# Performance work log

Measured on AMD Instinct MI355X. Metric: run time of the kernel, lower is better.

## Reference

```python
import jax, jax.numpy as jnp
import numpy as np

B, S, I, H, O, E, K = 2, 2048, 4096, 1376, 4096, 8, 2
BALANCE_W = 0.01  # balance_loss_weight in llama-moe


def setup_inputs() -> dict:
    key = jax.random.key(0)
    ks = jax.random.split(key, 6)
    sc = lambda k, shape, fan: jax.random.normal(k, shape, jnp.float32) * (fan ** -0.5)
    return {
        "x": jax.random.normal(ks[0], (B, S, I), jnp.float32),
        "gate_w": sc(ks[1], (E, I), I),          # linear gate network, no bias
        "w_gate": sc(ks[2], (E, H, I), I),       # GLU gate proj per expert
        "b_gate": jnp.zeros((E, H), jnp.float32),
        "w_up": sc(ks[3], (E, H, I), I),         # GLU up proj per expert
        "b_up": jnp.zeros((E, H), jnp.float32),
        "w_down": sc(ks[4], (E, O, H), H),       # down proj per expert
        "b_down": jnp.zeros((E, O), jnp.float32),
    }


def _cv_squared(v, eps=1e-10):
    # torch: x.var() / (x.mean()**2 + eps), unbiased variance
    mean = jnp.mean(v)
    var = jnp.sum((v - mean) ** 2) / (v.shape[0] - 1)
    return var / (mean ** 2 + eps)


def reference(x, gate_w, w_gate, b_gate, w_up, b_up, w_down, b_down):
    bsz, seq, _ = x.shape
    xt = x.reshape(-1, I)                         # [T, I] tokens
    T = xt.shape[0]

    # ---- TopKBalancedNoisyGate (no-noise branch) ----
    logits = xt @ gate_w.T                        # [T, E]
    top_logits, top_idx = jax.lax.top_k(logits, K)
    top_scores = jax.nn.softmax(top_logits, axis=-1)   # softmax over top-k logits
    # dense routing matrix: zeros.scatter(1, top_idx, top_scores)
    dense = jnp.zeros((T, E), xt.dtype).at[jnp.arange(T)[:, None], top_idx].set(top_scores)
    importance = dense.sum(axis=0)                # [E]
    load = (dense > 0).astype(jnp.float32).sum(axis=0)  # [E]
    gate_loss = BALANCE_W * (_cv_squared(importance) + _cv_squared(load))

    # ---- UniversalCalculator over LinearGLUExperts ----
    # Dense-dispatch formulation: compute every expert on every token, weight by
    # the (mostly-zero) routing matrix -> identical math to gather/grouped-GEMM/scatter.
    g = jnp.einsum('ti,ehi->teh', xt, w_gate) + b_gate        # [T, E, H]
    u = jnp.einsum('ti,ehi->teh', xt, w_up) + b_up            # [T, E, H]
    inter = jax.nn.silu(g) * u                                # GLU
    # score * (W_down h + b_down) == W_down (score*h) + score*b_down
    y = jnp.einsum('teh,eoh->to', inter * dense[:, :, None], w_down) + dense @ b_down
    return y.reshape(bsz, seq, O), gate_loss
```

## Files before the change

kernel.cpp:

```cpp
#include <hip/hip_runtime.h>
#include <hip/hip_bf16.h>
#include <stdint.h>

#define TN 4096
#define DI 4096
#define DH 1376
#define DHP 1408
#define DO 4096
#define NE 8
#define NPAIR 8192

typedef unsigned short u16;
typedef __bf16 bf16x8 __attribute__((ext_vector_type(8)));
typedef float f32x4 __attribute__((ext_vector_type(4)));
typedef uint32_t u32x4 __attribute__((ext_vector_type(4)));

__device__ __forceinline__ uint32_t pack2bf(float a, float b) {
    union { float f; uint32_t u; } ua, ub;
    ua.f = a; ub.f = b;
    uint32_t lo = (ua.u + 0x7fffu + ((ua.u >> 16) & 1u)) >> 16;
    uint32_t hi = (ub.u + 0x7fffu + ((ub.u >> 16) & 1u)) >> 16;
    return lo | (hi << 16);
}
__device__ __forceinline__ u16 f2bf(float a) {
    union { float f; uint32_t u; } ua; ua.f = a;
    return (u16)((ua.u + 0x7fffu + ((ua.u >> 16) & 1u)) >> 16);
}
__device__ __forceinline__ void gload16(const void* g, void* l) {
    __builtin_amdgcn_global_load_lds(
        (const __attribute__((address_space(1))) void*)g,
        (__attribute__((address_space(3))) void*)l, 16, 0, 0);
}
#define MEMFENCE() asm volatile("" ::: "memory")

__global__ __launch_bounds__(256) void k_cvt(const float* __restrict__ src,
                                             u16* __restrict__ dst, int n8)
{
    int i = blockIdx.x * 256 + threadIdx.x;
    if (i >= n8) return;
    const float4* s = (const float4*)(src + (size_t)i * 8);
    float4 a = s[0], b = s[1];
    u32x4 q = {pack2bf(a.x, a.y), pack2bf(a.z, a.w), pack2bf(b.x, b.y), pack2bf(b.z, b.w)};
    *(u32x4*)(dst + (size_t)i * 8) = q;
}

__global__ __launch_bounds__(256) void k_cvt_wd(const float* __restrict__ src,
                                                u16* __restrict__ dst)
{
    int i = blockIdx.x * 256 + threadIdx.x;
    int row = i / 176, c8 = (i % 176) * 8;
    u32x4 q = {0u, 0u, 0u, 0u};
    if (c8 < DH) {
        const float4* s = (const float4*)(src + (size_t)row * DH + c8);
        float4 a = s[0], b = s[1];
        q = (u32x4){pack2bf(a.x, a.y), pack2bf(a.z, a.w), pack2bf(b.x, b.y), pack2bf(b.z, b.w)};
    }
    *(u32x4*)(dst + (size_t)row * DHP + c8) = q;
}

__global__ __launch_bounds__(256) void k_gate(
    const float* __restrict__ x, const float* __restrict__ gw,
    u16* __restrict__ x16, int* __restrict__ tke, float* __restrict__ tks,
    int* __restrict__ cnt, float* __restrict__ imp)
{
    int t = blockIdx.x, tid = threadIdx.x;
    const float* xr = x + (size_t)t * DI;
    double acc[NE];
#pragma unroll
    for (int e = 0; e < NE; ++e) acc[e] = 0.0;
#pragma unroll
    for (int j = 0; j < 4; ++j) {
        int i4 = (j * 256 + tid) * 4;
        float4 xv = *(const float4*)(xr + i4);
        uint2 p; p.x = pack2bf(xv.x, xv.y); p.y = pack2bf(xv.z, xv.w);
        *(uint2*)(x16 + (size_t)t * DI + i4) = p;
#pragma unroll
        for (int e = 0; e < NE; ++e) {
            float4 wv = *(const float4*)(gw + (size_t)e * DI + i4);
            acc[e] = fma((double)xv.x, (double)wv.x, acc[e]);
            acc[e] = fma((double)xv.y, (double)wv.y, acc[e]);
            acc[e] = fma((double)xv.z, (double)wv.z, acc[e]);
            acc[e] = fma((double)xv.w, (double)wv.w, acc[e]);
        }
    }
#pragma unroll
    for (int o = 32; o > 0; o >>= 1)
#pragma unroll
        for (int e = 0; e < NE; ++e) acc[e] += __shfl_down(acc[e], o, 64);
    __shared__ double lred[4][NE];
    if ((tid & 63) == 0)
#pragma unroll
        for (int e = 0; e < NE; ++e) lred[tid >> 6][e] = acc[e];
    __syncthreads();
    if (tid == 0) {
        double lg[NE];
#pragma unroll
        for (int e = 0; e < NE; ++e) lg[e] = lred[0][e] + lred[1][e] + lred[2][e] + lred[3][e];
        int e1 = 0;
        for (int e = 1; e < NE; ++e) if (lg[e] > lg[e1]) e1 = e;
        int e2 = -1;
        for (int e = 0; e < NE; ++e) { if (e == e1) continue; if (e2 < 0 || lg[e] > lg[e2]) e2 = e; }
        float d = (float)(lg[e2] - lg[e1]);
        float ed = expf(d);
        float s1 = 1.0f / (1.0f + ed);
        float s2 = ed / (1.0f + ed);
        tke[2 * t] = e1; tke[2 * t + 1] = e2;
        tks[2 * t] = s1; tks[2 * t + 1] = s2;
        atomicAdd(&cnt[e1], 1); atomicAdd(&cnt[e2], 1);
        unsafeAtomicAdd(&imp[e1], s1); unsafeAtomicAdd(&imp[e2], s2);
    }
}

__global__ void k_finalize(const int* __restrict__ cnt, const float* __restrict__ imp,
                           int* __restrict__ off, float* __restrict__ loss_out)
{
    if (threadIdx.x == 0 && blockIdx.x == 0) {
        int o = 0;
        for (int e = 0; e < NE; ++e) { off[e] = o; o += cnt[e]; }
        float m1 = 0.f, m2 = 0.f;
        for (int e = 0; e < NE; ++e) { m1 += imp[e]; m2 += (float)cnt[e]; }
        m1 *= 0.125f; m2 *= 0.125f;
        float v1 = 0.f, v2 = 0.f;
        for (int e = 0; e < NE; ++e) {
            float d1 = imp[e] - m1, d2 = (float)cnt[e] - m2;
            v1 += d1 * d1; v2 += d2 * d2;
        }
        v1 /= 7.0f; v2 /= 7.0f;
        float cv1 = v1 / (m1 * m1 + 1e-10f);
        float cv2 = v2 / (m2 * m2 + 1e-10f);
        *loss_out = 0.01f * (cv1 + cv2);
    }
}

__global__ __launch_bounds__(256) void k_scatter(
    const int* __restrict__ tke, const float* __restrict__ tks,
    const int* __restrict__ off, int* __restrict__ fill,
    int* __restrict__ tok, float* __restrict__ sc)
{
    int t = blockIdx.x * 256 + threadIdx.x;
    if (t >= TN) return;
#pragma unroll
    for (int k = 0; k < 2; ++k) {
        int e = tke[2 * t + k];
        int pos = off[e] + atomicAdd(&fill[e], 1);
        tok[pos] = t; sc[pos] = tks[2 * t + k];
    }
}

__global__ __launch_bounds__(256) void k_yinit(
    const int* __restrict__ tke, const float* __restrict__ tks,
    const float* __restrict__ bd, float* __restrict__ y)
{
    int t = blockIdx.x, tid = threadIdx.x;
    int e1 = tke[2 * t], e2 = tke[2 * t + 1];
    float s1 = tks[2 * t], s2 = tks[2 * t + 1];
    const float4* b1 = (const float4*)(bd + (size_t)e1 * DO);
    const float4* b2 = (const float4*)(bd + (size_t)e2 * DO);
    float4* yr = (float4*)(y + (size_t)t * DO);
#pragma unroll
    for (int j = 0; j < 4; ++j) {
        int i = j * 256 + tid;
        float4 a = b1[i], b = b2[i], r;
        r.x = s1 * a.x + s2 * b.x; r.y = s1 * a.y + s2 * b.y;
        r.z = s1 * a.z + s2 * b.z; r.w = s1 * a.w + s2 * b.w;
        yr[i] = r;
    }
}


__global__ __launch_bounds__(256, 2) void k_stage1g(
    const u16* __restrict__ x16,
    const u16* __restrict__ wg16, const u16* __restrict__ wu16,
    const float* __restrict__ bg, const float* __restrict__ bu,
    const int* __restrict__ cnt, const int* __restrict__ off,
    const int* __restrict__ tok, const float* __restrict__ sc,
    u16* __restrict__ inter)
{
    int e = blockIdx.x & 7;
    int ce = cnt[e];
    int rows0 = (blockIdx.x >> 3) * 128;
    if (rows0 >= ce) return;
    int oe = off[e];
    int h0 = blockIdx.y * 128;
    int tid = threadIdx.x;

    __shared__ u16 As0[128 * 32]; __shared__ u16 As1[128 * 32]; __shared__ u16 As2[128 * 32];
    __shared__ u16 Gs0[128 * 32]; __shared__ u16 Gs1[128 * 32]; __shared__ u16 Gs2[128 * 32];
    __shared__ u16 Us0[128 * 32]; __shared__ u16 Us1[128 * 32]; __shared__ u16 Us2[128 * 32];

    int swz = ((tid & 3) ^ ((tid >> 3) & 3)) * 8;
    const u16* ab0; const u16* ab1; const u16* gb0; const u16* gb1;
    const u16* ub0; const u16* ub1;
    {
        int rl0 = tid >> 2, rl1 = 64 + (tid >> 2);
        int rg0 = oe + min(rows0 + rl0, ce - 1);
        int rg1 = oe + min(rows0 + rl1, ce - 1);
        ab0 = x16 + (size_t)tok[rg0] * DI + swz;
        ab1 = x16 + (size_t)tok[rg1] * DI + swz;
        int hr0 = min(h0 + rl0, DH - 1), hr1 = min(h0 + rl1, DH - 1);
        gb0 = wg16 + ((size_t)e * DH + hr0) * DI + swz;
        gb1 = wg16 + ((size_t)e * DH + hr1) * DI + swz;
        ub0 = wu16 + ((size_t)e * DH + hr0) * DI + swz;
        ub1 = wu16 + ((size_t)e * DH + hr1) * DI + swz;
    }

    int wid = tid >> 6, lane = tid & 63;
    int ldsw = wid * 512;
    int wm = wid >> 1, wn = wid & 1;
    int rA = wm * 64 + (lane & 15);
    int rB = wn * 64 + (lane & 15);
    int colb = (((lane >> 4) ^ ((lane >> 1) & 3)) & 3) * 8;

    f32x4 accg[4][4], accu[4][4];
    f32x4 vz = {0.f, 0.f, 0.f, 0.f};
#pragma unroll
    for (int m = 0; m < 4; ++m)
#pragma unroll
        for (int n = 0; n < 4; ++n) { accg[m][n] = vz; accu[m][n] = vz; }

#define S1_STAGE(A_, G_, U_, K0)                                   \
    do {                                                           \
        gload16(ab0 + (K0), &A_[ldsw]);                            \
        gload16(ab1 + (K0), &A_[2048 + ldsw]);                     \
        gload16(gb0 + (K0), &G_[ldsw]);                            \
        gload16(gb1 + (K0), &G_[2048 + ldsw]);                     \
        gload16(ub0 + (K0), &U_[ldsw]);                            \
        gload16(ub1 + (K0), &U_[2048 + ldsw]);                     \
    } while (0)

#define S1_COMPUTE(A_, G_, U_)                                     \
    do {                                                           \
        bf16x8 a[4], g[4], u[4];                                   \
        _Pragma("unroll")                                          \
        for (int m = 0; m < 4; ++m)                                \
            a[m] = *(const bf16x8*)&A_[(rA + m * 16) * 32 + colb]; \
        _Pragma("unroll")                                          \
        for (int n = 0; n < 4; ++n) {                              \
            g[n] = *(const bf16x8*)&G_[(rB + n * 16) * 32 + colb]; \
            u[n] = *(const bf16x8*)&U_[(rB + n * 16) * 32 + colb]; \
        }                                                          \
        __builtin_amdgcn_s_setprio(1);                             \
        _Pragma("unroll")                                          \
        for (int m = 0; m < 4; ++m)                                \
            _Pragma("unroll")                                      \
            for (int n = 0; n < 4; ++n) {                          \
                accg[m][n] = __builtin_amdgcn_mfma_f32_16x16x32_bf16(a[m], g[n], accg[m][n], 0, 0, 0); \
                accu[m][n] = __builtin_amdgcn_mfma_f32_16x16x32_bf16(a[m], u[n], accu[m][n], 0, 0, 0); \
            }                                                      \
        __builtin_amdgcn_s_setprio(0);                             \
    } while (0)

#define S1_PHASE(A_, G_, U_, KN)                                   \
    do {                                                           \
        asm volatile("s_waitcnt vmcnt(12)" ::: "memory");          \
        __builtin_amdgcn_s_barrier();                              \
        MEMFENCE();                                                \
        S1_COMPUTE(A_, G_, U_);                                    \
        __builtin_amdgcn_s_barrier();                              \
        MEMFENCE();                                                \
        S1_STAGE(A_, G_, U_, KN);                                  \
    } while (0)

    const int NT = DI / 32;
    const int KL = (NT - 1) * 32;
    S1_STAGE(As0, Gs0, Us0, 0);
    S1_STAGE(As1, Gs1, Us1, 32);
    S1_STAGE(As2, Gs2, Us2, 64);

    for (int kt = 0; kt + 4 < NT; kt += 3) {
        S1_PHASE(As0, Gs0, Us0, min((kt + 3) * 32, KL));
        S1_PHASE(As1, Gs1, Us1, min((kt + 4) * 32, KL));
        S1_PHASE(As2, Gs2, Us2, min((kt + 5) * 32, KL));
    }
    asm volatile("s_waitcnt vmcnt(12)" ::: "memory");
    __builtin_amdgcn_s_barrier();
    MEMFENCE();
    S1_COMPUTE(As0, Gs0, Us0);
    asm volatile("s_waitcnt vmcnt(6)" ::: "memory");
    __builtin_amdgcn_s_barrier();
    MEMFENCE();
    S1_COMPUTE(As1, Gs1, Us1);
    asm volatile("s_waitcnt vmcnt(0)" ::: "memory");
#undef S1_STAGE
#undef S1_COMPUTE
#undef S1_PHASE

    int rmax = ce - rows0;
    float bgv[4], buv[4];
    int hc[4]; bool hok[4];
#pragma unroll
    for (int n = 0; n < 4; ++n) {
        hc[n] = h0 + wn * 64 + n * 16 + (lane & 15);
        hok[n] = hc[n] < DH;
        bgv[n] = hok[n] ? bg[e * DH + hc[n]] : 0.f;
        buv[n] = hok[n] ? bu[e * DH + hc[n]] : 0.f;
    }
#pragma unroll
    for (int m = 0; m < 4; ++m) {
#pragma unroll
        for (int r = 0; r < 4; ++r) {
            int rl = wm * 64 + m * 16 + (lane >> 4) * 4 + r;
            if (rl < rmax) {
                int rg = oe + rows0 + rl;
                float s = sc[rg];
                size_t rowb = (size_t)rg * DHP;
#pragma unroll
                for (int n = 0; n < 4; ++n) {
                    float v = 0.f;
                    if (hok[n]) {
                        float gv = accg[m][n][r] + bgv[n];
                        float uv = accu[m][n][r] + buv[n];
                        float sig = 1.0f / (1.0f + __expf(-gv));
                        v = s * gv * sig * uv;
                    }
                    inter[rowb + hc[n]] = f2bf(v);
                }
            }
        }
    }
}

__global__ __launch_bounds__(256, 2) void k_stage2g(
    const u16* __restrict__ inter, const u16* __restrict__ wd16,
    const int* __restrict__ cnt, const int* __restrict__ off,
    const int* __restrict__ tok, float* __restrict__ y)
{
    int e = blockIdx.x & 7;
    int ce = cnt[e];
    int rows0 = (blockIdx.x >> 3) * 128;
    if (rows0 >= ce) return;
    int oe = off[e];
    int o0 = blockIdx.y * 128;
    int tid = threadIdx.x;

    __shared__ u16 As0[128 * 32]; __shared__ u16 As1[128 * 32]; __shared__ u16 As2[128 * 32];
    __shared__ u16 Bs0[128 * 32]; __shared__ u16 Bs1[128 * 32]; __shared__ u16 Bs2[128 * 32];

    int swz = ((tid & 3) ^ ((tid >> 3) & 3)) * 8;
    const u16* ab0; const u16* ab1; const u16* bb0; const u16* bb1;
    {
        int rl0 = tid >> 2, rl1 = 64 + (tid >> 2);
        int ar0 = min(oe + rows0 + rl0, NPAIR - 1);
        int ar1 = min(oe + rows0 + rl1, NPAIR - 1);
        ab0 = inter + (size_t)ar0 * DHP + swz;
        ab1 = inter + (size_t)ar1 * DHP + swz;
        bb0 = wd16 + ((size_t)e * DO + (o0 + rl0)) * DHP + swz;
        bb1 = wd16 + ((size_t)e * DO + (o0 + rl1)) * DHP + swz;
    }

    int wid = tid >> 6, lane = tid & 63;
    int ldsw = wid * 512;
    int wm = wid >> 1, wn = wid & 1;
    int rA = wm * 64 + (lane & 15);
    int rB = wn * 64 + (lane & 15);
    int colb = (((lane >> 4) ^ ((lane >> 1) & 3)) & 3) * 8;

    f32x4 acc[4][4];
    f32x4 vz = {0.f, 0.f, 0.f, 0.f};
#pragma unroll
    for (int m = 0; m < 4; ++m)
#pragma unroll
        for (int n = 0; n < 4; ++n) acc[m][n] = vz;

#define S2_STAGE(A_, B_, K0)                                       \
    do {                                                           \
        gload16(ab0 + (K0), &A_[ldsw]);                            \
        gload16(ab1 + (K0), &A_[2048 + ldsw]);                     \
        gload16(bb0 + (K0), &B_[ldsw]);                            \
        gload16(bb1 + (K0), &B_[2048 + ldsw]);                     \
    } while (0)

#define S2_COMPUTE(A_, B_)                                         \
    do {                                                           \
        bf16x8 a[4], b[4];                                         \
        _Pragma("unroll")                                          \
        for (int m = 0; m < 4; ++m)                                \
            a[m] = *(const bf16x8*)&A_[(rA + m * 16) * 32 + colb]; \
        _Pragma("unroll")                                          \
        for (int n = 0; n < 4; ++n)                                \
            b[n] = *(const bf16x8*)&B_[(rB + n * 16) * 32 + colb]; \
        __builtin_amdgcn_s_setprio(1);                             \
        _Pragma("unroll")                                          \
        for (int m = 0; m < 4; ++m)                                \
            _Pragma("unroll")                                      \
            for (int n = 0; n < 4; ++n)                            \
                acc[m][n] = __builtin_amdgcn_mfma_f32_16x16x32_bf16(a[m], b[n], acc[m][n], 0, 0, 0); \
        __builtin_amdgcn_s_setprio(0);                             \
    } while (0)

#define S2_PHASE(A_, B_, KN)                                       \
    do {                                                           \
        asm volatile("s_waitcnt vmcnt(8)" ::: "memory");           \
        __builtin_amdgcn_s_barrier();                              \
        MEMFENCE();                                                \
        S2_COMPUTE(A_, B_);                                        \
        __builtin_amdgcn_s_barrier();                              \
        MEMFENCE();                                                \
        S2_STAGE(A_, B_, KN);                                      \
    } while (0)

    const int NT = DHP / 32;
    const int KL = (NT - 1) * 32;
    S2_STAGE(As0, Bs0, 0);
    S2_STAGE(As1, Bs1, 32);
    S2_STAGE(As2, Bs2, 64);

    for (int kt = 0; kt + 4 < NT; kt += 3) {
        S2_PHASE(As0, Bs0, min((kt + 3) * 32, KL));
        S2_PHASE(As1, Bs1, min((kt + 4) * 32, KL));
        S2_PHASE(As2, Bs2, min((kt + 5) * 32, KL));
    }
    asm volatile("s_waitcnt vmcnt(8)" ::: "memory");
    __builtin_amdgcn_s_barrier();
    MEMFENCE();
    S2_COMPUTE(As0, Bs0);
    asm volatile("s_waitcnt vmcnt(4)" ::: "memory");
    __builtin_amdgcn_s_barrier();
    MEMFENCE();
    S2_COMPUTE(As1, Bs1);
    asm volatile("s_waitcnt vmcnt(0)" ::: "memory");
#undef S2_STAGE
#undef S2_COMPUTE
#undef S2_PHASE

    int rmax = ce - rows0;
#pragma unroll
    for (int m = 0; m < 4; ++m) {
#pragma unroll
        for (int r = 0; r < 4; ++r) {
            int rl = wm * 64 + m * 16 + (lane >> 4) * 4 + r;
            if (rl >= rmax) continue;
            int t = tok[oe + rows0 + rl];
            float* yr = y + (size_t)t * DO + o0 + wn * 64 + (lane & 15);
#pragma unroll
            for (int n = 0; n < 4; ++n)
                unsafeAtomicAdd(yr + n * 16, acc[m][n][r]);
        }
    }
}

extern "C" void kernel_launch(void* const* d_in, const int* in_sizes, int n_in,
                              void* d_out, int out_size, void* d_ws, size_t ws_size,
                              hipStream_t stream)
{
    const float* x  = (const float*)d_in[0];
    const float* gw = (const float*)d_in[1];
    const float* wg = (const float*)d_in[2];
    const float* bg = (const float*)d_in[3];
    const float* wu = (const float*)d_in[4];
    const float* bu = (const float*)d_in[5];
    const float* wd = (const float*)d_in[6];
    const float* bd = (const float*)d_in[7];
    float* y = (float*)d_out;
    float* loss = y + (size_t)TN * DO;

    uint8_t* ws = (uint8_t*)d_ws;
    u16*   x16   = (u16*)(ws + 0);
    u16*   inter = (u16*)(ws + 33554432ull);
    u16*   wg16  = (u16*)(ws + 56623104ull);
    u16*   wu16  = (u16*)(ws + 146800640ull);
    u16*   wd16  = (u16*)(ws + 236978176ull);
    int*   tok   = (int*)(ws + 329252864ull);
    float* sc    = (float*)(ws + 329285632ull);
    int*   tke   = (int*)(ws + 329318400ull);
    float* tks   = (float*)(ws + 329351168ull);
    int*   misc  = (int*)(ws + 329383936ull);
    int* cnt = misc; int* fill = misc + 8; int* off = misc + 16;
    float* imp = (float*)(misc + 24);

    hipMemsetAsync(misc, 0, 128, stream);
    k_cvt<<<22016, 256, 0, stream>>>(wg, wg16, 5636096);
    k_cvt<<<22016, 256, 0, stream>>>(wu, wu16, 5636096);
    k_cvt_wd<<<22528, 256, 0, stream>>>(wd, wd16);
    k_gate<<<TN, 256, 0, stream>>>(x, gw, x16, tke, tks, cnt, imp);
    k_finalize<<<1, 64, 0, stream>>>(cnt, imp, off, loss);
    k_scatter<<<TN / 256, 256, 0, stream>>>(tke, tks, off, fill, tok, sc);
    k_yinit<<<TN, 256, 0, stream>>>(tke, tks, bd, y);
    k_stage1g<<<dim3(256, 11), 256, 0, stream>>>(x16, wg16, wu16, bg, bu, cnt, off, tok, sc, inter);
    k_stage2g<<<dim3(256, 32), 256, 0, stream>>>(inter, wd16, cnt, off, tok, y);
}
```

Before: 793.4 us.

## Fuse conversion, gating, scatter kernels and fold down-proj bias into GEMM

Merges the three weight conversion kernels with the gating kernel into one launch, merges finalize into scatter, and drops the y-init kernel. y is now memset to zero and the down-projection bias is folded in as an extra K column: the routing score goes into the padded inter column and the bias into the matching padded weight column. Stage-2 pipelining drops from triple to double LDS buffering. This cuts launch count and a full pass over y, at the cost of shallower prefetch in the down-projection GEMM.

```diff
diff --git a/kernel.cpp b/kernel.cpp
--- a/kernel.cpp
+++ b/kernel.cpp
@@ -33,90 +33,102 @@
 }
 #define MEMFENCE() asm volatile("" ::: "memory")
 
-__global__ __launch_bounds__(256) void k_cvt(const float* __restrict__ src,
-                                             u16* __restrict__ dst, int n8)
-{
-    int i = blockIdx.x * 256 + threadIdx.x;
-    if (i >= n8) return;
-    const float4* s = (const float4*)(src + (size_t)i * 8);
-    float4 a = s[0], b = s[1];
-    u32x4 q = {pack2bf(a.x, a.y), pack2bf(a.z, a.w), pack2bf(b.x, b.y), pack2bf(b.z, b.w)};
-    *(u32x4*)(dst + (size_t)i * 8) = q;
-}
-
-__global__ __launch_bounds__(256) void k_cvt_wd(const float* __restrict__ src,
-                                                u16* __restrict__ dst)
-{
-    int i = blockIdx.x * 256 + threadIdx.x;
-    int row = i / 176, c8 = (i % 176) * 8;
-    u32x4 q = {0u, 0u, 0u, 0u};
-    if (c8 < DH) {
-        const float4* s = (const float4*)(src + (size_t)row * DH + c8);
-        float4 a = s[0], b = s[1];
-        q = (u32x4){pack2bf(a.x, a.y), pack2bf(a.z, a.w), pack2bf(b.x, b.y), pack2bf(b.z, b.w)};
-    }
-    *(u32x4*)(dst + (size_t)row * DHP + c8) = q;
-}
-
-__global__ __launch_bounds__(256) void k_gate(
+__global__ __launch_bounds__(256) void k_cvt_gate(
     const float* __restrict__ x, const float* __restrict__ gw,
-    u16* __restrict__ x16, int* __restrict__ tke, float* __restrict__ tks,
+    const float* __restrict__ wg, const float* __restrict__ wu,
+    const float* __restrict__ wd, const float* __restrict__ bd,
+    u16* __restrict__ x16, u16* __restrict__ wg16, u16* __restrict__ wu16,
+    u16* __restrict__ wd16,
+    int* __restrict__ tke, float* __restrict__ tks,
     int* __restrict__ cnt, float* __restrict__ imp)
 {
-    int t = blockIdx.x, tid = threadIdx.x;
-    const float* xr = x + (size_t)t * DI;
-    double acc[NE];
-#pragma unroll
-    for (int e = 0; e < NE; ++e) acc[e] = 0.0;
-#pragma unroll
-    for (int j = 0; j < 4; ++j) {
-        int i4 = (j * 256 + tid) * 4;
-        float4 xv = *(const float4*)(xr + i4);
-        uint2 p; p.x = pack2bf(xv.x, xv.y); p.y = pack2bf(xv.z, xv.w);
-        *(uint2*)(x16 + (size_t)t * DI + i4) = p;
-#pragma unroll
-        for (int e = 0; e < NE; ++e) {
-            float4 wv = *(const float4*)(gw + (size_t)e * DI + i4);
-            acc[e] = fma((double)xv.x, (double)wv.x, acc[e]);
-            acc[e] = fma((double)xv.y, (double)wv.y, acc[e]);
-            acc[e] = fma((double)xv.z, (double)wv.z, acc[e]);
-            acc[e] = fma((double)xv.w, (double)wv.w, acc[e]);
-        }
-    }
-#pragma unroll
-    for (int o = 32; o > 0; o >>= 1)
-#pragma unroll
-        for (int e = 0; e < NE; ++e) acc[e] += __shfl_down(acc[e], o, 64);
-    __shared__ double lred[4][NE];
-    if ((tid & 63) == 0)
-#pragma unroll
-        for (int e = 0; e < NE; ++e) lred[tid >> 6][e] = acc[e];
-    __syncthreads();
-    if (tid == 0) {
-        double lg[NE];
-#pragma unroll
-        for (int e = 0; e < NE; ++e) lg[e] = lred[0][e] + lred[1][e] + lred[2][e] + lred[3][e];
-        int e1 = 0;
-        for (int e = 1; e < NE; ++e) if (lg[e] > lg[e1]) e1 = e;
-        int e2 = -1;
-        for (int e = 0; e < NE; ++e) { if (e == e1) continue; if (e2 < 0 || lg[e] > lg[e2]) e2 = e; }
-        float d = (float)(lg[e2] - lg[e1]);
-        float ed = expf(d);
-        float s1 = 1.0f / (1.0f + ed);
-        float s2 = ed / (1.0f + ed);
-        tke[2 * t] = e1; tke[2 * t + 1] = e2;
-        tks[2 * t] = s1; tks[2 * t + 1] = s2;
-        atomicAdd(&cnt[e1], 1); atomicAdd(&cnt[e2], 1);
-        unsafeAtomicAdd(&imp[e1], s1); unsafeAtomicAdd(&imp[e2], s2);
-    }
-}
-
-__global__ void k_finalize(const int* __restrict__ cnt, const float* __restrict__ imp,
-                           int* __restrict__ off, float* __restrict__ loss_out)
+    int tid = threadIdx.x;
+    if (blockIdx.x < TN) {
+        int t = blockIdx.x;
+        const float* xr = x + (size_t)t * DI;
+        double acc[NE];
+#pragma unroll
+        for (int e = 0; e < NE; ++e) acc[e] = 0.0;
+#pragma unroll
+        for (int j = 0; j < 4; ++j) {
+            int i4 = (j * 256 + tid) * 4;
+            float4 xv = *(const float4*)(xr + i4);
+            uint2 p; p.x = pack2bf(xv.x, xv.y); p.y = pack2bf(xv.z, xv.w);
+            *(uint2*)(x16 + (size_t)t * DI + i4) = p;
+#pragma unroll
+            for (int e = 0; e < NE; ++e) {
+                float4 wv = *(const float4*)(gw + (size_t)e * DI + i4);
+                acc[e] = fma((double)xv.x, (double)wv.x, acc[e]);
+                acc[e] = fma((double)xv.y, (double)wv.y, acc[e]);
+                acc[e] = fma((double)xv.z, (double)wv.z, acc[e]);
+                acc[e] = fma((double)xv.w, (double)wv.w, acc[e]);
+            }
+        }
+#pragma unroll
+        for (int o = 32; o > 0; o >>= 1)
+#pragma unroll
+            for (int e = 0; e < NE; ++e) acc[e] += __shfl_down(acc[e], o, 64);
+        __shared__ double lred[4][NE];
+        if ((tid & 63) == 0)
+#pragma unroll
+            for (int e = 0; e < NE; ++e) lred[tid >> 6][e] = acc[e];
+        __syncthreads();
+        if (tid == 0) {
+            double lg[NE];
+#pragma unroll
+            for (int e = 0; e < NE; ++e) lg[e] = lred[0][e] + lred[1][e] + lred[2][e] + lred[3][e];
+            int e1 = 0;
+            for (int e = 1; e < NE; ++e) if (lg[e] > lg[e1]) e1 = e;
+            int e2 = -1;
+            for (int e = 0; e < NE; ++e) { if (e == e1) continue; if (e2 < 0 || lg[e] > lg[e2]) e2 = e; }
+            float d = (float)(lg[e2] - lg[e1]);
+            float ed = expf(d);
+            float s1 = 1.0f / (1.0f + ed);
+            float s2 = ed / (1.0f + ed);
+            tke[2 * t] = e1; tke[2 * t + 1] = e2;
+            tks[2 * t] = s1; tks[2 * t + 1] = s2;
+            atomicAdd(&cnt[e1], 1); atomicAdd(&cnt[e2], 1);
+            unsafeAtomicAdd(&imp[e1], s1); unsafeAtomicAdd(&imp[e2], s2);
+        }
+        return;
+    }
+    int i = (blockIdx.x - TN) * 256 + tid;
+    if (i < 11272192) {
+        const float* src = (i < 5636096) ? wg : wu;
+        u16* dst = (i < 5636096) ? wg16 : wu16;
+        int j = (i < 5636096) ? i : i - 5636096;
+        const float4* s = (const float4*)(src + (size_t)j * 8);
+        float4 a = s[0], b = s[1];
+        u32x4 v = {pack2bf(a.x, a.y), pack2bf(a.z, a.w), pack2bf(b.x, b.y), pack2bf(b.z, b.w)};
+        *(u32x4*)(dst + (size_t)j * 8) = v;
+    } else {
+        int j = i - 11272192;
+        if (j >= 5767168) return;
+        int row = j / 176, c8 = (j % 176) * 8;
+        u32x4 v = {0u, 0u, 0u, 0u};
+        if (c8 < DH) {
+            const float4* s = (const float4*)(wd + (size_t)row * DH + c8);
+            float4 a = s[0], b = s[1];
+            v = (u32x4){pack2bf(a.x, a.y), pack2bf(a.z, a.w), pack2bf(b.x, b.y), pack2bf(b.z, b.w)};
+        } else if (c8 == DH) {
+            v.x = (uint32_t)f2bf(bd[row]);
+        }
+        *(u32x4*)(wd16 + (size_t)row * DHP + c8) = v;
+    }
+}
+
+__global__ __launch_bounds__(256) void k_scatter_fin(
+    const int* __restrict__ tke, const float* __restrict__ tks,
+    const int* __restrict__ cnt, const float* __restrict__ imp,
+    int* __restrict__ off, int* __restrict__ fill,
+    int* __restrict__ tok, float* __restrict__ sc, float* __restrict__ loss_out)
 {
-    if (threadIdx.x == 0 && blockIdx.x == 0) {
-        int o = 0;
-        for (int e = 0; e < NE; ++e) { off[e] = o; o += cnt[e]; }
+    int loc[NE]; int o = 0;
+#pragma unroll
+    for (int e = 0; e < NE; ++e) { loc[e] = o; o += cnt[e]; }
+    if (blockIdx.x == 0 && threadIdx.x == 0) {
+#pragma unroll
+        for (int e = 0; e < NE; ++e) off[e] = loc[e];
         float m1 = 0.f, m2 = 0.f;
         for (int e = 0; e < NE; ++e) { m1 += imp[e]; m2 += (float)cnt[e]; }
         m1 *= 0.125f; m2 *= 0.125f;
@@ -126,47 +138,17 @@
             v1 += d1 * d1; v2 += d2 * d2;
         }
         v1 /= 7.0f; v2 /= 7.0f;
-        float cv1 = v1 / (m1 * m1 + 1e-10f);
-        float cv2 = v2 / (m2 * m2 + 1e-10f);
-        *loss_out = 0.01f * (cv1 + cv2);
-    }
-}
-
-__global__ __launch_bounds__(256) void k_scatter(
-    const int* __restrict__ tke, const float* __restrict__ tks,
-    const int* __restrict__ off, int* __restrict__ fill,
-    int* __restrict__ tok, float* __restrict__ sc)
-{
+        *loss_out = 0.01f * (v1 / (m1 * m1 + 1e-10f) + v2 / (m2 * m2 + 1e-10f));
+    }
     int t = blockIdx.x * 256 + threadIdx.x;
     if (t >= TN) return;
 #pragma unroll
     for (int k = 0; k < 2; ++k) {
         int e = tke[2 * t + k];
-        int pos = off[e] + atomicAdd(&fill[e], 1);
+        int pos = loc[e] + atomicAdd(&fill[e], 1);
         tok[pos] = t; sc[pos] = tks[2 * t + k];
     }
 }
-
-__global__ __launch_bounds__(256) void k_yinit(
-    const int* __restrict__ tke, const float* __restrict__ tks,
-    const float* __restrict__ bd, float* __restrict__ y)
-{
-    int t = blockIdx.x, tid = threadIdx.x;
-    int e1 = tke[2 * t], e2 = tke[2 * t + 1];
-    float s1 = tks[2 * t], s2 = tks[2 * t + 1];
-    const float4* b1 = (const float4*)(bd + (size_t)e1 * DO);
-    const float4* b2 = (const float4*)(bd + (size_t)e2 * DO);
-    float4* yr = (float4*)(y + (size_t)t * DO);
-#pragma unroll
-    for (int j = 0; j < 4; ++j) {
-        int i = j * 256 + tid;
-        float4 a = b1[i], b = b2[i], r;
-        r.x = s1 * a.x + s2 * b.x; r.y = s1 * a.y + s2 * b.y;
-        r.z = s1 * a.z + s2 * b.z; r.w = s1 * a.w + s2 * b.w;
-        yr[i] = r;
-    }
-}
-
 
 __global__ __launch_bounds__(256, 2) void k_stage1g(
     const u16* __restrict__ x16,
@@ -312,6 +294,8 @@
                         float uv = accu[m][n][r] + buv[n];
                         float sig = 1.0f / (1.0f + __expf(-gv));
                         v = s * gv * sig * uv;
+                    } else if (hc[n] == DH) {
+                        v = s;
                     }
                     inter[rowb + hc[n]] = f2bf(v);
                 }
@@ -320,7 +304,7 @@
     }
 }
 
-__global__ __launch_bounds__(256, 2) void k_stage2g(
+__global__ __launch_bounds__(256, 2) void k_stage2h(
     const u16* __restrict__ inter, const u16* __restrict__ wd16,
     const int* __restrict__ cnt, const int* __restrict__ off,
     const int* __restrict__ tok, float* __restrict__ y)
@@ -333,8 +317,8 @@
     int o0 = blockIdx.y * 128;
     int tid = threadIdx.x;
 
-    __shared__ u16 As0[128 * 32]; __shared__ u16 As1[128 * 32]; __shared__ u16 As2[128 * 32];
-    __shared__ u16 Bs0[128 * 32]; __shared__ u16 Bs1[128 * 32]; __shared__ u16 Bs2[128 * 32];
+    __shared__ u16 As0[128 * 32]; __shared__ u16 As1[128 * 32];
+    __shared__ u16 Bs0[128 * 32]; __shared__ u16 Bs1[128 * 32];
 
     int swz = ((tid & 3) ^ ((tid >> 3) & 3)) * 8;
     const u16* ab0; const u16* ab1; const u16* bb0; const u16* bb1;
@@ -388,40 +372,36 @@
         __builtin_amdgcn_s_setprio(0);                             \
     } while (0)
 
-#define S2_PHASE(A_, B_, KN)                                       \
-    do {                                                           \
-        asm volatile("s_waitcnt vmcnt(8)" ::: "memory");           \
-        __builtin_amdgcn_s_barrier();                              \
-        MEMFENCE();                                                \
-        S2_COMPUTE(A_, B_);                                        \
-        __builtin_amdgcn_s_barrier();                              \
-        MEMFENCE();                                                \
-        S2_STAGE(A_, B_, KN);                                      \
-    } while (0)
-
     const int NT = DHP / 32;
-    const int KL = (NT - 1) * 32;
     S2_STAGE(As0, Bs0, 0);
     S2_STAGE(As1, Bs1, 32);
-    S2_STAGE(As2, Bs2, 64);
-
-    for (int kt = 0; kt + 4 < NT; kt += 3) {
-        S2_PHASE(As0, Bs0, min((kt + 3) * 32, KL));
-        S2_PHASE(As1, Bs1, min((kt + 4) * 32, KL));
-        S2_PHASE(As2, Bs2, min((kt + 5) * 32, KL));
-    }
-    asm volatile("s_waitcnt vmcnt(8)" ::: "memory");
+
+    for (int kt = 0; kt < NT - 2; kt += 2) {
+        asm volatile("s_waitcnt vmcnt(4)" ::: "memory");
+        __builtin_amdgcn_s_barrier();
+        MEMFENCE();
+        S2_COMPUTE(As0, Bs0);
+        __builtin_amdgcn_s_barrier();
+        MEMFENCE();
+        S2_STAGE(As0, Bs0, (kt + 2) * 32);
+        asm volatile("s_waitcnt vmcnt(4)" ::: "memory");
+        __builtin_amdgcn_s_barrier();
+        MEMFENCE();
+        S2_COMPUTE(As1, Bs1);
+        __builtin_amdgcn_s_barrier();
+        MEMFENCE();
+        S2_STAGE(As1, Bs1, (kt + 3) * 32);
+    }
+    asm volatile("s_waitcnt vmcnt(4)" ::: "memory");
     __builtin_amdgcn_s_barrier();
     MEMFENCE();
     S2_COMPUTE(As0, Bs0);
-    asm volatile("s_waitcnt vmcnt(4)" ::: "memory");
+    asm volatile("s_waitcnt vmcnt(0)" ::: "memory");
     __builtin_amdgcn_s_barrier();
     MEMFENCE();
     S2_COMPUTE(As1, Bs1);
-    asm volatile("s_waitcnt vmcnt(0)" ::: "memory");
 #undef S2_STAGE
 #undef S2_COMPUTE
-#undef S2_PHASE
 
     int rmax = ce - rows0;
 #pragma unroll
@@ -469,13 +449,11 @@
     float* imp = (float*)(misc + 24);
 
     hipMemsetAsync(misc, 0, 128, stream);
-    k_cvt<<<22016, 256, 0, stream>>>(wg, wg16, 5636096);
-    k_cvt<<<22016, 256, 0, stream>>>(wu, wu16, 5636096);
-    k_cvt_wd<<<22528, 256, 0, stream>>>(wd, wd16);
-    k_gate<<<TN, 256, 0, stream>>>(x, gw, x16, tke, tks, cnt, imp);
-    k_finalize<<<1, 64, 0, stream>>>(cnt, imp, off, loss);
-    k_scatter<<<TN / 256, 256, 0, stream>>>(tke, tks, off, fill, tok, sc);
-    k_yinit<<<TN, 256, 0, stream>>>(tke, tks, bd, y);
+    hipMemsetAsync(d_out, 0, (size_t)out_size * 4, stream);
+    k_cvt_gate<<<70656, 256, 0, stream>>>(x, gw, wg, wu, wd, bd,
+                                          x16, wg16, wu16, wd16,
+                                          tke, tks, cnt, imp);
+    k_scatter_fin<<<16, 256, 0, stream>>>(tke, tks, cnt, imp, off, fill, tok, sc, loss);
     k_stage1g<<<dim3(256, 11), 256, 0, stream>>>(x16, wg16, wu16, bg, bu, cnt, off, tok, sc, inter);
-    k_stage2g<<<dim3(256, 32), 256, 0, stream>>>(inter, wd16, cnt, off, tok, y);
-}
+    k_stage2h<<<dim3(256, 32), 256, 0, stream>>>(inter, wd16, cnt, off, tok, y);
+}
```

After: 787.2 us. Within noise of the previous version (-0.8%).
